# Optimization experiments

Hardware: AMD Instinct MI355X
Metric: run time of the kernel (lower is better)

Reference implementation:

```python
import jax, jax.numpy as jnp
import numpy as np

B, N, D = 8, 64, 512          # batch, latent tokens, token dim
C, H, W, P = 256, 128, 128, 36  # img feat channels/HW, sampling points
PG = 128                       # parameter-generator inner dim (0.25*D)
HEADS = 8                      # D // 64
TOT = C * C + P * P            # adaptive mixing param count per token


def _ln(x, g, b):
    m = x.mean(-1, keepdims=True)
    v = x.var(-1, keepdims=True)
    return (x - m) / jnp.sqrt(v + 1e-5) * g + b


def _gelu(x):
    return jax.nn.gelu(x, approximate=False)


def _grid_sample(img, grid):
    # img: (B,C,H,W); grid: (B,N,P,2) in [-1,1]; bilinear, border pad, align_corners=False
    Bi, Ci, Hi, Wi = img.shape
    x = ((grid[..., 0] + 1.0) * Wi - 1.0) * 0.5
    y = ((grid[..., 1] + 1.0) * Hi - 1.0) * 0.5
    x0 = jnp.floor(x)
    y0 = jnp.floor(y)
    wx = x - x0
    wy = y - y0
    x0i = jnp.clip(x0.astype(jnp.int32), 0, Wi - 1)
    x1i = jnp.clip(x0.astype(jnp.int32) + 1, 0, Wi - 1)
    y0i = jnp.clip(y0.astype(jnp.int32), 0, Hi - 1)
    y1i = jnp.clip(y0.astype(jnp.int32) + 1, 0, Hi - 1)
    imgt = img.transpose(0, 2, 3, 1)  # (B,H,W,C)
    bidx = jnp.arange(Bi)[:, None, None]
    v00 = imgt[bidx, y0i, x0i]  # (B,N,P,C)
    v01 = imgt[bidx, y0i, x1i]
    v10 = imgt[bidx, y1i, x0i]
    v11 = imgt[bidx, y1i, x1i]
    wx = wx[..., None]
    wy = wy[..., None]
    return (v00 * (1 - wx) * (1 - wy) + v01 * wx * (1 - wy)
            + v10 * (1 - wx) * wy + v11 * wx * wy)


def setup_inputs() -> dict:
    key = jax.random.key(0)
    ks = jax.random.split(key, 16)
    rn = lambda k, s, sc: jax.random.normal(k, s, jnp.float32) * sc
    tl = jax.random.uniform(ks[0], (B, N, 2), jnp.float32) * 0.5
    wh = 0.2 + jax.random.uniform(ks[1], (B, N, 2), jnp.float32) * 0.4
    return dict(
        token_embed=rn(ks[2], (B, N, D), 1.0),
        token_roi=jnp.concatenate([tl, tl + wh], axis=-1),
        img_feat=rn(ks[3], (B, C, H, W), 1.0),
        ln_off_g=jnp.ones(D), ln_off_b=jnp.zeros(D),
        w_off=rn(ks[4], (D, P * 2), D ** -0.5),
        roi_offset_bias=rn(ks[5], (P * 2,), 1.0),
        ln_pg_g=jnp.ones(D), ln_pg_b=jnp.zeros(D),
        w_pg1=rn(ks[6], (D, PG), D ** -0.5), b_pg1=jnp.zeros(PG),
        w_pg2=rn(ks[7], (PG, TOT), 0.02 * PG ** -0.5),
        b_pg2=rn(ks[8], (TOT,), 0.02),
        m_beta=jnp.zeros(C), s_beta=jnp.zeros(P),
        w_out=rn(ks[9], (P * C, D), (P * C) ** -0.5), b_out=jnp.zeros(D),
        ln1_g=jnp.ones(D), ln1_b=jnp.zeros(D),
        w_qkv=rn(ks[10], (D, 3 * D), D ** -0.5), b_qkv=jnp.zeros(3 * D),
        w_proj=rn(ks[11], (D, D), D ** -0.5), b_proj=jnp.zeros(D),
        ln2_g=jnp.ones(D), ln2_b=jnp.zeros(D),
        w_fc1=rn(ks[12], (D, 4 * D), D ** -0.5), b_fc1=jnp.zeros(4 * D),
        w_fc2=rn(ks[13], (4 * D, D), (4 * D) ** -0.5), b_fc2=jnp.zeros(D),
    )


def reference(token_embed, token_roi, img_feat,
              ln_off_g, ln_off_b, w_off, roi_offset_bias,
              ln_pg_g, ln_pg_b, w_pg1, b_pg1, w_pg2, b_pg2,
              m_beta, s_beta, w_out, b_out,
              ln1_g, ln1_b, w_qkv, b_qkv, w_proj, b_proj,
              ln2_g, ln2_b, w_fc1, b_fc1, w_fc2, b_fc2):
    Bq, Nq, Dm = token_embed.shape
    # --- OP.SAMPLING_M: offsets -> absolute points (n_heads=1) ---
    off = _ln(token_embed, ln_off_g, ln_off_b) @ w_off + roi_offset_bias  # (B,N,2P)
    off = off.reshape(Bq, Nq, 1, P, 2)
    mu = off.mean(-2, keepdims=True)
    sd = jnp.std(off, axis=-2, keepdims=True, ddof=1) + 1e-5  # unbiased, as torch.std
    off = (off - mu) / (3.0 * sd)
    xy = (token_roi[..., 2:] + token_roi[..., :2]) * 0.5
    wh = token_roi[..., 2:] - token_roi[..., :2]
    pts = xy[:, :, None, None, :] + off * wh[:, :, None, None, :]  # (B,N,1,P,2)
    grid = pts.reshape(Bq, Nq, P, 2) * 2.0 - 1.0
    sampled = _grid_sample(img_feat, grid)  # (B,N,P,C)
    # --- adaptive mixing (AdaMixer): per-token generated channel/spatial weights ---
    q = _ln(token_embed, ln_pg_g, ln_pg_b)
    params = (q @ w_pg1 + b_pg1) @ w_pg2 + b_pg2  # (B,N,TOT)
    cm = params[..., :C * C].reshape(Bq, Nq, C, C)
    sm = params[..., C * C:].reshape(Bq, Nq, P, P)
    h = _gelu(jnp.einsum('bnpc,bncd->bnpd', sampled, cm) + m_beta)
    h = _gelu(jnp.einsum('bnqp,bnpd->bnqd', sm, h) + s_beta[:, None])
    token_embed = token_embed + (h.reshape(Bq, Nq, P * C) @ w_out + b_out)
    # --- OP.ATTN ---
    x = _ln(token_embed, ln1_g, ln1_b)
    hd = Dm // HEADS
    qkv = (x @ w_qkv + b_qkv).reshape(Bq, Nq, 3, HEADS, hd)
    qh, kh, vh = qkv[:, :, 0], qkv[:, :, 1], qkv[:, :, 2]
    att = jax.nn.softmax(jnp.einsum('bqhd,bkhd->bhqk', qh, kh) * hd ** -0.5, axis=-1)
    o = jnp.einsum('bhqk,bkhd->bqhd', att, vh).reshape(Bq, Nq, Dm)
    token_embed = token_embed + (o @ w_proj + b_proj)
    # --- OP.MLP ---
    x = _ln(token_embed, ln2_g, ln2_b)
    token_embed = token_embed + (_gelu(x @ w_fc1 + b_fc1) @ w_fc2 + b_fc2)
    return token_embed
```

## Files before the change

### kernel.cpp

```cpp
#include <hip/hip_runtime.h>
#include <hip/hip_bf16.h>

typedef __hip_bfloat16 bf16;
typedef __attribute__((ext_vector_type(8))) short short8;
typedef __attribute__((ext_vector_type(4))) short s16x4;
typedef __attribute__((ext_vector_type(4))) float f32x4;

#define NTOK 512
#define TOTC 66832
#define CM_SZ 65536

__device__ __forceinline__ float b2f(bf16 x) { return __bfloat162float(x); }
__device__ __forceinline__ bf16 f2b(float x) { return __float2bfloat16(x); }
__device__ __forceinline__ float gelu_f(float x) {
  return 0.5f * x * (1.0f + erff(x * 0.7071067811865476f));
}
__device__ __forceinline__ f32x4 mfma16(short8 a, short8 b, f32x4 c) {
  return __builtin_amdgcn_mfma_f32_16x16x32_bf16(a, b, c, 0, 0, 0);
}

__global__ __launch_bounds__(256) void k_head(
    const float* __restrict__ te, const float* __restrict__ roi,
    const float* __restrict__ g_off, const float* __restrict__ b_off,
    const float* __restrict__ w_off, const float* __restrict__ off_bias,
    const float* __restrict__ g_pg, const float* __restrict__ b_pg,
    const float* __restrict__ w_pg1, const float* __restrict__ b_pg1,
    bf16* __restrict__ t_out, int* __restrict__ meta_i, float* __restrict__ meta_w,
    const float* __restrict__ img, bf16* __restrict__ imgT,
    const float* __restrict__ w0, bf16* __restrict__ o0,
    const float* __restrict__ w1, bf16* __restrict__ o1,
    const float* __restrict__ w2, bf16* __restrict__ o2,
    const float* __restrict__ w3, bf16* __restrict__ o3,
    const float* __restrict__ w4, bf16* __restrict__ o4) {
  __shared__ __align__(16) char smem_raw[36864];
  int blk = blockIdx.x;
  int t = threadIdx.x;
  if (blk < 512) {
    int tok = blk;
    int lane = t & 63, w = t >> 6;
    float* xo = (float*)smem_raw;
    float* xq = xo + 512;
    float* offb = xq + 512;
    float* red = offb + 72;
    float* wsum = red + 4;
    size_t base = (size_t)tok * 512;
    float a0 = te[base + t];
    float a1 = te[base + t + 256];
    float s = a0 + a1;
#pragma unroll
    for (int o = 32; o; o >>= 1) s += __shfl_xor(s, o);
    if (lane == 0) wsum[w] = s;
    __syncthreads();
    float mean = (wsum[0] + wsum[1] + wsum[2] + wsum[3]) * (1.0f / 512.0f);
    float d0 = a0 - mean, d1 = a1 - mean;
    float ss = d0 * d0 + d1 * d1;
#pragma unroll
    for (int o = 32; o; o >>= 1) ss += __shfl_xor(ss, o);
    __syncthreads();
    if (lane == 0) wsum[w] = ss;
    __syncthreads();
    float var = (wsum[0] + wsum[1] + wsum[2] + wsum[3]) * (1.0f / 512.0f);
    float rstd = rsqrtf(var + 1e-5f);
    xo[t] = d0 * rstd * g_off[t] + b_off[t];
    xo[t + 256] = d1 * rstd * g_off[t + 256] + b_off[t + 256];
    xq[t] = d0 * rstd * g_pg[t] + b_pg[t];
    xq[t + 256] = d1 * rstd * g_pg[t + 256] + b_pg[t + 256];
    __syncthreads();
    if (t < 128) {
      float acc = b_pg1[t];
      for (int d = 0; d < 512; ++d) acc = fmaf(xq[d], w_pg1[d * 128 + t], acc);
      t_out[(size_t)tok * 128 + t] = f2b(acc);
    } else if (t < 200) {
      int j = t - 128;
      float acc = off_bias[j];
      for (int d = 0; d < 512; ++d) acc = fmaf(xo[d], w_off[d * 72 + j], acc);
      offb[j] = acc;
    }
    __syncthreads();
    if (t < 2) {
      float mu = 0.f;
      for (int p = 0; p < 36; ++p) mu += offb[p * 2 + t];
      mu *= (1.0f / 36.0f);
      float s2 = 0.f;
      for (int p = 0; p < 36; ++p) { float dd = offb[p * 2 + t] - mu; s2 += dd * dd; }
      float sd = sqrtf(s2 * (1.0f / 35.0f)) + 1e-5f;
      red[t] = mu;
      red[2 + t] = 1.0f / (3.0f * sd);
    }
    __syncthreads();
    if (t < 36) {
      int p = t;
      float r0 = roi[tok * 4 + 0], r1 = roi[tok * 4 + 1];
      float r2 = roi[tok * 4 + 2], r3 = roi[tok * 4 + 3];
      float cx = (r0 + r2) * 0.5f, cy = (r1 + r3) * 0.5f;
      float bw = r2 - r0, bh = r3 - r1;
      float ox = (offb[p * 2 + 0] - red[0]) * red[2];
      float oy = (offb[p * 2 + 1] - red[1]) * red[3];
      float fx = (cx + ox * bw) * 128.0f - 0.5f;
      float fy = (cy + oy * bh) * 128.0f - 0.5f;
      float x0f = floorf(fx), y0f = floorf(fy);
      float wx = fx - x0f, wy = fy - y0f;
      int x0 = min(max((int)x0f, 0), 127);
      int x1 = min(max((int)x0f + 1, 0), 127);
      int y0 = min(max((int)y0f, 0), 127);
      int y1 = min(max((int)y0f + 1, 0), 127);
      int ibase = (tok >> 6) * 16384;
      int mi = (tok * 36 + p) * 4;
      meta_i[mi + 0] = (ibase + y0 * 128 + x0) * 256;
      meta_i[mi + 1] = (ibase + y0 * 128 + x1) * 256;
      meta_i[mi + 2] = (ibase + y1 * 128 + x0) * 256;
      meta_i[mi + 3] = (ibase + y1 * 128 + x1) * 256;
      meta_w[mi + 0] = (1.f - wx) * (1.f - wy);
      meta_w[mi + 1] = wx * (1.f - wy);
      meta_w[mi + 2] = (1.f - wx) * wy;
      meta_w[mi + 3] = wx * wy;
    }
  } else if (blk < 2560) {
    int bb = blk - 512;
    int b = bb >> 8;
    int hw0 = (bb & 255) * 64;
    bf16 (*tl)[72] = (bf16(*)[72])smem_raw;
    int hw_l = (t & 15) * 4;
#pragma unroll
    for (int pass = 0; pass < 16; ++pass) {
      int c = (t >> 4) + 16 * pass;
      const float4 v = *(const float4*)&img[((size_t)(b * 256 + c) << 14) + hw0 + hw_l];
      float vv[4] = {v.x, v.y, v.z, v.w};
      int mask = ((c >> 3) & 31) << 1;
      int base = hw_l ^ (mask & 60);
      int swp = mask & 2;
      bf16 o[4];
#pragma unroll
      for (int k = 0; k < 4; ++k) o[k] = f2b(vv[k ^ swp]);
      *(s16x4*)&tl[c][base] = *(const s16x4*)o;
    }
    __syncthreads();
    int c8 = (t & 31) * 8;
    int hwb = t >> 5;
    int rmask = ((c8 >> 3) & 31) << 1;
#pragma unroll
    for (int pass = 0; pass < 8; ++pass) {
      int hw = hwb + 8 * pass;
      bf16 tmp[8];
#pragma unroll
      for (int j = 0; j < 8; ++j) tmp[j] = tl[c8 + j][hw ^ rmask];
      *(short8*)&imgT[((size_t)(b << 14) + hw0 + hw) * 256 + c8] = *(const short8*)tmp;
    }
  } else {
    int b = blk - 2560;
    const float* W;
    bf16* O;
    int K, N, loc;
    if (b < 4608) { W = w0; O = o0; K = 9216; N = 512; loc = b; }
    else if (b < 5376) { W = w1; O = o1; K = 512; N = 1536; loc = b - 4608; }
    else if (b < 5632) { W = w2; O = o2; K = 512; N = 512; loc = b - 5376; }
    else if (b < 6656) { W = w3; O = o3; K = 512; N = 2048; loc = b - 5632; }
    else { W = w4; O = o4; K = 2048; N = 512; loc = b - 6656; }
    int ntn = N >> 5;
    int nb = loc % ntn, kb = loc / ntn;
    int n0 = nb * 32, k0 = kb * 32;
    float (*tw)[33] = (float(*)[33])smem_raw;
    int r = t >> 5, c = t & 31;
#pragma unroll
    for (int i = 0; i < 4; ++i)
      tw[r + 8 * i][c] = W[(size_t)(k0 + r + 8 * i) * N + n0 + c];
    __syncthreads();
    int n_l = t >> 3, k4 = (t & 7) * 4;
    bf16 tmp[4];
#pragma unroll
    for (int j = 0; j < 4; ++j) tmp[j] = f2b(tw[k4 + j][n_l]);
    *(s16x4*)&O[(size_t)(n0 + n_l) * K + k0 + k4] = *(const s16x4*)tmp;
  }
}

__global__ __launch_bounds__(256) void k_samp_pg2(
    const bf16* __restrict__ tb16, const float* __restrict__ w2,
    const float* __restrict__ b2, bf16* __restrict__ pchunk,
    const bf16* __restrict__ imgT, const int* __restrict__ meta_i,
    const float* __restrict__ meta_w, bf16* __restrict__ S) {
  __shared__ bf16 BsT[64][136];
  __shared__ bf16 stg[64][72];
  int blk = blockIdx.x;
  int t = threadIdx.x;
  if (blk < 1045) {
    int n0 = blk * 64;
    int lane = t & 63, w = t >> 6;
    int quad = lane >> 4, l16 = lane & 15;
    {
      int nl = (t & 15) * 4, kk = t >> 4;
#pragma unroll
      for (int pass = 0; pass < 8; ++pass) {
        int k = kk + pass * 16;
        int n = n0 + nl;
        int nc = (n + 3 < TOTC) ? n : (TOTC - 4);
        const float4 v = *(const float4*)(w2 + (size_t)k * TOTC + nc);
        BsT[nl + 0][k] = f2b(v.x);
        BsT[nl + 1][k] = f2b(v.y);
        BsT[nl + 2][k] = f2b(v.z);
        BsT[nl + 3][k] = f2b(v.w);
      }
    }
    __syncthreads();
    float bias_r[4];
#pragma unroll
    for (int nt = 0; nt < 4; ++nt) {
      int col = n0 + nt * 16 + l16;
      bias_r[nt] = (col < TOTC) ? b2[col] : 0.f;
    }
    for (int half = 0; half < 2; ++half) {
      int row0 = half * 256;
      f32x4 acc[4][4];
#pragma unroll
      for (int i = 0; i < 4; ++i)
#pragma unroll
        for (int j = 0; j < 4; ++j) acc[i][j] = (f32x4){0.f, 0.f, 0.f, 0.f};
      const bf16* Abase = tb16 + ((size_t)(row0 + w * 64 + l16)) * 128 + quad * 8;
#pragma unroll
      for (int ks = 0; ks < 4; ++ks) {
        short8 af[4], bff[4];
#pragma unroll
        for (int mt = 0; mt < 4; ++mt)
          af[mt] = *(const short8*)(Abase + mt * 16 * 128 + ks * 32);
#pragma unroll
        for (int nt = 0; nt < 4; ++nt)
          bff[nt] = *(const short8*)(&BsT[nt * 16 + l16][ks * 32 + quad * 8]);
#pragma unroll
        for (int mt = 0; mt < 4; ++mt)
#pragma unroll
          for (int nt = 0; nt < 4; ++nt)
            acc[mt][nt] = mfma16(af[mt], bff[nt], acc[mt][nt]);
      }
#pragma unroll
      for (int mt = 0; mt < 4; ++mt) {
        __syncthreads();
#pragma unroll
        for (int nt = 0; nt < 4; ++nt)
#pragma unroll
          for (int r = 0; r < 4; ++r)
            stg[w * 16 + quad * 4 + r][nt * 16 + l16] =
                f2b(acc[mt][nt][r] + bias_r[nt]);
        __syncthreads();
#pragma unroll
        for (int pass = 0; pass < 2; ++pass) {
          int t2 = t + pass * 256;
          int row_l = t2 >> 3;
          int wi = row_l >> 4, rr = row_l & 15;
          int c8 = (t2 & 7) * 8;
          int col = n0 + c8;
          if (col < TOTC) {
            int grow = row0 + wi * 64 + mt * 16 + rr;
            *(short8*)&pchunk[(size_t)grow * TOTC + col] =
                *(const short8*)&stg[wi * 16 + rr][c8];
          }
        }
      }
      __syncthreads();
    }
  } else {
    int tok = blk - 1045;
#pragma unroll 6
    for (int p = 0; p < 36; ++p) {
      int mi = (tok * 36 + p) * 4;
      int o00 = meta_i[mi + 0], o01 = meta_i[mi + 1], o10 = meta_i[mi + 2], o11 = meta_i[mi + 3];
      float w00 = meta_w[mi + 0], w01 = meta_w[mi + 1], w10 = meta_w[mi + 2], w11 = meta_w[mi + 3];
      float v = w00 * b2f(imgT[o00 + t]) + w01 * b2f(imgT[o01 + t]) +
                w10 * b2f(imgT[o10 + t]) + w11 * b2f(imgT[o11 + t]);
      S[((size_t)tok * 36 + p) * 256 + t] = f2b(v);
    }
  }
}

__global__ __launch_bounds__(256) void k_mix3(const bf16* __restrict__ pchunk,
                                              const bf16* __restrict__ S,
                                              const float* __restrict__ m_beta,
                                              const float* __restrict__ s_beta,
                                              bf16* __restrict__ h2) {
  int tok = blockIdx.x, dh = blockIdx.y * 128;
  int t = threadIdx.x, lane = t & 63, w = t >> 6;
  int quad = lane >> 4, l16 = lane & 15;
  __shared__ bf16 h1T[128][72];
  __shared__ bf16 smS[48][72];
  __shared__ short cmw[4][32][40];
  for (int i = t; i < 1728; i += 256) ((unsigned*)smS)[i] = 0u;
  __syncthreads();
  const bf16* sm = pchunk + (size_t)tok * TOTC + CM_SZ;
  for (int i = t; i < 1296; i += 256) {
    int q = i / 36, p = i - q * 36;
    smS[q][p] = sm[i];
  }
  f32x4 acc[3][2];
#pragma unroll
  for (int i = 0; i < 3; ++i)
#pragma unroll
    for (int j = 0; j < 2; ++j) acc[i][j] = (f32x4){0.f, 0.f, 0.f, 0.f};
  const bf16* Sg = S + (size_t)tok * 9216;
  const bf16* Cg = pchunk + (size_t)tok * TOTC;
  int dw = w * 32;
  int c_l = lane & 31;
  int dtop = (lane >> 5) * 16;
  const bf16* src0 = Cg + (size_t)c_l * 256 + dh + dw + dtop;
  short8 v0 = *(const short8*)src0;
  short8 v1 = *(const short8*)(src0 + 8);
#pragma unroll
  for (int kc = 0; kc < 256; kc += 32) {
#pragma unroll
    for (int j = 0; j < 8; ++j) cmw[w][dtop + j][c_l] = v0[j];
#pragma unroll
    for (int j = 0; j < 8; ++j) cmw[w][dtop + 8 + j][c_l] = v1[j];
    short8 a[3];
#pragma unroll
    for (int mt = 0; mt < 3; ++mt)
      a[mt] = *(const short8*)(Sg + (size_t)(mt * 16 + l16) * 256 + kc + quad * 8);
    short8 v0n, v1n;
    if (kc < 224) {
      const bf16* srcn = Cg + (size_t)(kc + 32 + c_l) * 256 + dh + dw + dtop;
      v0n = *(const short8*)srcn;
      v1n = *(const short8*)(srcn + 8);
    }
    asm volatile("" ::: "memory");
    short8 bfr[2];
#pragma unroll
    for (int nt = 0; nt < 2; ++nt)
      bfr[nt] = *(const short8*)&cmw[w][nt * 16 + l16][quad * 8];
#pragma unroll
    for (int mt = 0; mt < 3; ++mt)
#pragma unroll
      for (int nt = 0; nt < 2; ++nt)
        acc[mt][nt] = mfma16(a[mt], bfr[nt], acc[mt][nt]);
    asm volatile("" ::: "memory");
    v0 = v0n;
    v1 = v1n;
  }
#pragma unroll
  for (int nt = 0; nt < 2; ++nt) {
    int dl = dw + nt * 16 + l16;
    float mb = m_beta[dh + dl];
#pragma unroll
    for (int mt = 0; mt < 3; ++mt)
#pragma unroll
      for (int r = 0; r < 4; ++r) {
        int p = mt * 16 + quad * 4 + r;
        if (p < 36) h1T[dl][p] = f2b(gelu_f(acc[mt][nt][r] + mb));
      }
  }
  for (int i = t; i < 128 * 28; i += 256) {
    int d = i / 28, p = 36 + i % 28;
    h1T[d][p] = (bf16)0.f;
  }
  __syncthreads();
  f32x4 acc2[3][2];
#pragma unroll
  for (int i = 0; i < 3; ++i)
#pragma unroll
    for (int j = 0; j < 2; ++j) acc2[i][j] = (f32x4){0.f, 0.f, 0.f, 0.f};
#pragma unroll
  for (int ks = 0; ks < 2; ++ks) {
    short8 a2[3], b2v[2];
#pragma unroll
    for (int mt = 0; mt < 3; ++mt)
      a2[mt] = *(const short8*)&smS[mt * 16 + l16][ks * 32 + quad * 8];
#pragma unroll
    for (int nt = 0; nt < 2; ++nt)
      b2v[nt] = *(const short8*)&h1T[dw + nt * 16 + l16][ks * 32 + quad * 8];
#pragma unroll
    for (int mt = 0; mt < 3; ++mt)
#pragma unroll
      for (int nt = 0; nt < 2; ++nt)
        acc2[mt][nt] = mfma16(a2[mt], b2v[nt], acc2[mt][nt]);
  }
  bf16* h2p = h2 + (size_t)tok * 9216 + dh;
#pragma unroll
  for (int mt = 0; mt < 3; ++mt)
#pragma unroll
    for (int r = 0; r < 4; ++r) {
      int q = mt * 16 + quad * 4 + r;
      if (q >= 36) continue;
      float sb = s_beta[q];
#pragma unroll
      for (int nt = 0; nt < 2; ++nt)
        h2p[q * 256 + dw + nt * 16 + l16] = f2b(gelu_f(acc2[mt][nt][r] + sb));
    }
}

__global__ __launch_bounds__(256) void k_gemm_bt(const bf16* __restrict__ A,
                                                 const bf16* __restrict__ BT,
                                                 float* __restrict__ part,
                                                 int M, int N, int K) {
  int nb = blockIdx.x, mb = blockIdx.y, ks = blockIdx.z;
  int kchunk = K / gridDim.z;
  int k0 = ks * kchunk;
  __shared__ bf16 As[64][72], Bs[64][72];
  int t = threadIdx.x, lane = t & 63, w = t >> 6;
  int quad = lane >> 4, l16 = lane & 15;
  int wm = (w >> 1) * 32, wn = (w & 1) * 32;
  int r = t >> 2, kk = (t & 3) * 16;
  f32x4 acc[2][2];
#pragma unroll
  for (int i = 0; i < 2; ++i)
#pragma unroll
    for (int j = 0; j < 2; ++j) acc[i][j] = (f32x4){0.f, 0.f, 0.f, 0.f};
  for (int kt = 0; kt < kchunk; kt += 64) {
    __syncthreads();
    const bf16* ga = A + (size_t)(mb * 64 + r) * K + k0 + kt + kk;
    *(short8*)&As[r][kk] = *(const short8*)ga;
    *(short8*)&As[r][kk + 8] = *(const short8*)(ga + 8);
    const bf16* gb = BT + (size_t)(nb * 64 + r) * K + k0 + kt + kk;
    *(short8*)&Bs[r][kk] = *(const short8*)gb;
    *(short8*)&Bs[r][kk + 8] = *(const short8*)(gb + 8);
    __syncthreads();
#pragma unroll
    for (int kss = 0; kss < 2; ++kss) {
      short8 af[2], bff[2];
#pragma unroll
      for (int mt = 0; mt < 2; ++mt)
        af[mt] = *(const short8*)&As[wm + mt * 16 + l16][kss * 32 + quad * 8];
#pragma unroll
      for (int nt = 0; nt < 2; ++nt)
        bff[nt] = *(const short8*)&Bs[wn + nt * 16 + l16][kss * 32 + quad * 8];
#pragma unroll
      for (int mt = 0; mt < 2; ++mt)
#pragma unroll
        for (int nt = 0; nt < 2; ++nt)
          acc[mt][nt] = mfma16(af[mt], bff[nt], acc[mt][nt]);
    }
  }
#pragma unroll
  for (int mt = 0; mt < 2; ++mt)
#pragma unroll
    for (int rr = 0; rr < 4; ++rr) {
      int m = mb * 64 + wm + mt * 16 + quad * 4 + rr;
#pragma unroll
      for (int nt = 0; nt < 2; ++nt) {
        int n = nb * 64 + wn + nt * 16 + l16;
        part[(size_t)ks * M * N + (size_t)m * N + n] = acc[mt][nt][rr];
      }
    }
}

__global__ __launch_bounds__(256) void k_gemm_ep(const bf16* __restrict__ A,
                                                 const bf16* __restrict__ BT,
                                                 const float* __restrict__ bias,
                                                 int M, int N, int K, int do_gelu,
                                                 const float* __restrict__ resf,
                                                 float* __restrict__ outf,
                                                 bf16* __restrict__ outh) {
  int nb = blockIdx.x, mb = blockIdx.y;
  __shared__ bf16 As[64][72], Bs[64][72];
  int t = threadIdx.x, lane = t & 63, w = t >> 6;
  int quad = lane >> 4, l16 = lane & 15;
  int wm = (w >> 1) * 32, wn = (w & 1) * 32;
  int r = t >> 2, kk = (t & 3) * 16;
  f32x4 acc[2][2];
#pragma unroll
  for (int i = 0; i < 2; ++i)
#pragma unroll
    for (int j = 0; j < 2; ++j) acc[i][j] = (f32x4){0.f, 0.f, 0.f, 0.f};
  for (int kt = 0; kt < K; kt += 64) {
    __syncthreads();
    const bf16* ga = A + (size_t)(mb * 64 + r) * K + kt + kk;
    *(short8*)&As[r][kk] = *(const short8*)ga;
    *(short8*)&As[r][kk + 8] = *(const short8*)(ga + 8);
    const bf16* gb = BT + (size_t)(nb * 64 + r) * K + kt + kk;
    *(short8*)&Bs[r][kk] = *(const short8*)gb;
    *(short8*)&Bs[r][kk + 8] = *(const short8*)(gb + 8);
    __syncthreads();
#pragma unroll
    for (int kss = 0; kss < 2; ++kss) {
      short8 af[2], bff[2];
#pragma unroll
      for (int mt = 0; mt < 2; ++mt)
        af[mt] = *(const short8*)&As[wm + mt * 16 + l16][kss * 32 + quad * 8];
#pragma unroll
      for (int nt = 0; nt < 2; ++nt)
        bff[nt] = *(const short8*)&Bs[wn + nt * 16 + l16][kss * 32 + quad * 8];
#pragma unroll
      for (int mt = 0; mt < 2; ++mt)
#pragma unroll
        for (int nt = 0; nt < 2; ++nt)
          acc[mt][nt] = mfma16(af[mt], bff[nt], acc[mt][nt]);
    }
  }
#pragma unroll
  for (int mt = 0; mt < 2; ++mt)
#pragma unroll
    for (int rr = 0; rr < 4; ++rr) {
      int m = mb * 64 + wm + mt * 16 + quad * 4 + rr;
#pragma unroll
      for (int nt = 0; nt < 2; ++nt) {
        int n = nb * 64 + wn + nt * 16 + l16;
        float a = acc[mt][nt][rr] + bias[n];
        if (resf) a += resf[(size_t)m * N + n];
        if (do_gelu) a = gelu_f(a);
        if (outf) outf[(size_t)m * N + n] = a;
        else outh[(size_t)m * N + n] = f2b(a);
      }
    }
}

__global__ __launch_bounds__(256) void k_epi_ln(const float* __restrict__ part, int S_,
                                                const float* __restrict__ bias,
                                                const float* __restrict__ res,
                                                const float* __restrict__ g,
                                                const float* __restrict__ bvec,
                                                float* __restrict__ xout,
                                                bf16* __restrict__ lnout) {
  int tok = blockIdx.x, t = threadIdx.x, lane = t & 63, w = t >> 6;
  __shared__ float wsum[4];
  size_t base = (size_t)tok * 512;
  float a0 = bias[t] + res[base + t];
  float a1 = bias[t + 256] + res[base + t + 256];
  for (int sp = 0; sp < S_; ++sp) {
    const float* p = part + (size_t)sp * 262144 + base;
    a0 += p[t];
    a1 += p[t + 256];
  }
  xout[base + t] = a0;
  xout[base + t + 256] = a1;
  float s = a0 + a1;
#pragma unroll
  for (int o = 32; o; o >>= 1) s += __shfl_xor(s, o);
  if (lane == 0) wsum[w] = s;
  __syncthreads();
  float mean = (wsum[0] + wsum[1] + wsum[2] + wsum[3]) * (1.0f / 512.0f);
  float d0 = a0 - mean, d1 = a1 - mean;
  float ss = d0 * d0 + d1 * d1;
#pragma unroll
  for (int o = 32; o; o >>= 1) ss += __shfl_xor(ss, o);
  __syncthreads();
  if (lane == 0) wsum[w] = ss;
  __syncthreads();
  float var = (wsum[0] + wsum[1] + wsum[2] + wsum[3]) * (1.0f / 512.0f);
  float rstd = rsqrtf(var + 1e-5f);
  lnout[base + t] = f2b(d0 * rstd * g[t] + bvec[t]);
  lnout[base + t + 256] = f2b(d1 * rstd * g[t + 256] + bvec[t + 256]);
}

__global__ __launch_bounds__(256) void k_attn(const float* __restrict__ qkvf,
                                              bf16* __restrict__ obuf) {
  int b = blockIdx.x >> 3, h = blockIdx.x & 7;
  int q0 = blockIdx.y * 16;
  __shared__ float kT[64][65];
  __shared__ float vT[64][65];
  __shared__ float att[16][65];
  int t = threadIdx.x, lane = t & 63, w = t >> 6;
#pragma unroll
  for (int i = 0; i < 16; ++i) {
    int idx = t + i * 256;
    int j = idx >> 6, d = idx & 63;
    size_t tb = (size_t)(b * 64 + j) * 1536 + h * 64 + d;
    kT[j][d] = qkvf[tb + 512];
    vT[j][d] = qkvf[tb + 1024];
  }
  __syncthreads();
#pragma unroll
  for (int m = 0; m < 4; ++m) {
    int il = w * 4 + m;
    int i = q0 + il;
    const float* qrow = &qkvf[(size_t)(b * 64 + i) * 1536 + h * 64];
    float s = 0.f;
    for (int d = 0; d < 64; ++d) s = fmaf(qrow[d], kT[lane][d], s);
    s *= 0.125f;
    float mx = s;
#pragma unroll
    for (int o = 32; o; o >>= 1) mx = fmaxf(mx, __shfl_xor(mx, o));
    float e = expf(s - mx);
    float sum = e;
#pragma unroll
    for (int o = 32; o; o >>= 1) sum += __shfl_xor(sum, o);
    att[il][lane] = e / sum;
  }
  __syncthreads();
#pragma unroll
  for (int m = 0; m < 4; ++m) {
    int il = w * 4 + m;
    int i = q0 + il;
    float o = 0.f;
    for (int j = 0; j < 64; ++j) o = fmaf(att[il][j], vT[j][lane], o);
    obuf[(size_t)(b * 64 + i) * 512 + h * 64 + lane] = f2b(o);
  }
}

extern "C" void kernel_launch(void* const* d_in, const int* in_sizes, int n_in,
                              void* d_out, int out_size, void* d_ws, size_t ws_size,
                              hipStream_t stream) {
  const float* te = (const float*)d_in[0];
  const float* roi = (const float*)d_in[1];
  const float* img = (const float*)d_in[2];
  const float* ln_off_g = (const float*)d_in[3];
  const float* ln_off_b = (const float*)d_in[4];
  const float* w_off = (const float*)d_in[5];
  const float* off_bias = (const float*)d_in[6];
  const float* ln_pg_g = (const float*)d_in[7];
  const float* ln_pg_b = (const float*)d_in[8];
  const float* w_pg1 = (const float*)d_in[9];
  const float* b_pg1 = (const float*)d_in[10];
  const float* w_pg2 = (const float*)d_in[11];
  const float* b_pg2 = (const float*)d_in[12];
  const float* m_beta = (const float*)d_in[13];
  const float* s_beta = (const float*)d_in[14];
  const float* w_out = (const float*)d_in[15];
  const float* b_out = (const float*)d_in[16];
  const float* ln1_g = (const float*)d_in[17];
  const float* ln1_b = (const float*)d_in[18];
  const float* w_qkv = (const float*)d_in[19];
  const float* b_qkv = (const float*)d_in[20];
  const float* w_proj = (const float*)d_in[21];
  const float* b_proj = (const float*)d_in[22];
  const float* ln2_g = (const float*)d_in[23];
  const float* ln2_b = (const float*)d_in[24];
  const float* w_fc1 = (const float*)d_in[25];
  const float* b_fc1 = (const float*)d_in[26];
  const float* w_fc2 = (const float*)d_in[27];
  const float* b_fc2 = (const float*)d_in[28];

  char* ws = (char*)d_ws;
  bf16* imgT = (bf16*)ws;
  char* ov = ws;
  bf16* h2 = (bf16*)ov; ov += 9437184;
  float* part = (float*)ov; ov += 8388608;
  float* x1 = (float*)ov; ov += 1048576;
  float* xa = (float*)ov; ov += 1048576;
  float* qkvf = (float*)ov; ov += 3145728;
  bf16* ln1buf = (bf16*)ov; ov += 524288;
  bf16* ln2buf = (bf16*)ov; ov += 524288;
  bf16* obuf = (bf16*)ov; ov += 524288;
  bf16* hfc = (bf16*)ov; ov += 2097152;
  char* tail = ws + 67108864;
  bf16* Sbuf = (bf16*)tail; tail += 9437184;
  bf16* tb16 = (bf16*)tail; tail += 131072;
  int* meta_i = (int*)tail; tail += 294912;
  float* meta_w = (float*)tail; tail += 294912;
  bf16* pchunk = (bf16*)tail; tail += (size_t)NTOK * TOTC * 2;
  bf16* w_outT = (bf16*)tail; tail += 9437184;
  bf16* w_qkvT = (bf16*)tail; tail += 1572864;
  bf16* w_projT = (bf16*)tail; tail += 524288;
  bf16* w_fc1T = (bf16*)tail; tail += 2097152;
  bf16* w_fc2T = (bf16*)tail; tail += 2097152;
  (void)ws_size;

  k_head<<<10240, 256, 0, stream>>>(te, roi, ln_off_g, ln_off_b, w_off, off_bias,
                                    ln_pg_g, ln_pg_b, w_pg1, b_pg1, tb16, meta_i, meta_w,
                                    img, imgT,
                                    w_out, w_outT, w_qkv, w_qkvT, w_proj, w_projT,
                                    w_fc1, w_fc1T, w_fc2, w_fc2T);
  k_samp_pg2<<<1557, 256, 0, stream>>>(tb16, w_pg2, b_pg2, pchunk,
                                       imgT, meta_i, meta_w, Sbuf);
  k_mix3<<<dim3(512, 2), 256, 0, stream>>>(pchunk, Sbuf, m_beta, s_beta, h2);

  k_gemm_bt<<<dim3(8, 8, 8), 256, 0, stream>>>(h2, w_outT, part, 512, 512, 9216);
  k_epi_ln<<<512, 256, 0, stream>>>(part, 8, b_out, te, ln1_g, ln1_b, x1, ln1buf);

  k_gemm_ep<<<dim3(24, 8), 256, 0, stream>>>(ln1buf, w_qkvT, b_qkv, 512, 1536, 512, 0,
                                             nullptr, qkvf, nullptr);
  k_attn<<<dim3(64, 4), 256, 0, stream>>>(qkvf, obuf);
  k_gemm_bt<<<dim3(8, 8, 4), 256, 0, stream>>>(obuf, w_projT, part, 512, 512, 512);
  k_epi_ln<<<512, 256, 0, stream>>>(part, 4, b_proj, x1, ln2_g, ln2_b, xa, ln2buf);

  k_gemm_ep<<<dim3(32, 8), 256, 0, stream>>>(ln2buf, w_fc1T, b_fc1, 512, 2048, 512, 1,
                                             nullptr, nullptr, hfc);
  k_gemm_ep<<<dim3(8, 8), 256, 0, stream>>>(hfc, w_fc2T, b_fc2, 512, 512, 2048, 0,
                                            xa, (float*)d_out, nullptr);
}
```

Baseline: 487.4 us.

## Split image transpose into its own kernel and split-K the final FC2 GEMM

Moves the NCHW-to-NHWC bf16 image transpose out of the fused head kernel into a dedicated 1024-thread kernel with a 256x256 shared tile. This lets the head kernel drop its large shared-memory buffer, which should raise occupancy for the LN and weight-transpose blocks. The FC2 GEMM (K=2048, only 64 blocks) is changed to a split-K GEMM writing partials, followed by a new elementwise epilogue kernel that adds bias and residual. The cost is an extra kernel launch and an extra round trip of the partial sums through memory.

```diff
diff --git a/kernel.cpp b/kernel.cpp
--- a/kernel.cpp
+++ b/kernel.cpp
@@ -17,6 +17,40 @@
 }
 __device__ __forceinline__ f32x4 mfma16(short8 a, short8 b, f32x4 c) {
   return __builtin_amdgcn_mfma_f32_16x16x32_bf16(a, b, c, 0, 0, 0);
+}
+
+__global__ __launch_bounds__(1024) void k_imgT(const float* __restrict__ img,
+                                               bf16* __restrict__ imgT) {
+  __shared__ bf16 tl[256][256];
+  int t = threadIdx.x;
+  int b = blockIdx.y;
+  int hw0 = blockIdx.x * 256;
+  int lane4 = (t & 63) * 4;
+#pragma unroll
+  for (int pass = 0; pass < 16; ++pass) {
+    int c = (t >> 6) + 16 * pass;
+    const float4 v = *(const float4*)&img[((size_t)(b * 256 + c) << 14) + hw0 + lane4];
+    float vv[4] = {v.x, v.y, v.z, v.w};
+    int mask = ((c >> 3) & 31) << 1;
+    int base = lane4 ^ (mask & 60);
+    int swp = mask & 2;
+    bf16 o[4];
+#pragma unroll
+    for (int k = 0; k < 4; ++k) o[k] = f2b(vv[k ^ swp]);
+    *(s16x4*)&tl[c][base] = *(const s16x4*)o;
+  }
+  __syncthreads();
+  int c8 = (t & 31) * 8;
+  int hwb = t >> 5;
+  int rmask = ((c8 >> 3) & 31) << 1;
+#pragma unroll
+  for (int pass = 0; pass < 8; ++pass) {
+    int hw = hwb + 32 * pass;
+    bf16 tmp[8];
+#pragma unroll
+    for (int j = 0; j < 8; ++j) tmp[j] = tl[c8 + j][hw ^ rmask];
+    *(short8*)&imgT[((size_t)(b << 14) + hw0 + hw) * 256 + c8] = *(const short8*)tmp;
+  }
 }
 
 __global__ __launch_bounds__(256) void k_head(
@@ -26,13 +60,12 @@
     const float* __restrict__ g_pg, const float* __restrict__ b_pg,
     const float* __restrict__ w_pg1, const float* __restrict__ b_pg1,
     bf16* __restrict__ t_out, int* __restrict__ meta_i, float* __restrict__ meta_w,
-    const float* __restrict__ img, bf16* __restrict__ imgT,
     const float* __restrict__ w0, bf16* __restrict__ o0,
     const float* __restrict__ w1, bf16* __restrict__ o1,
     const float* __restrict__ w2, bf16* __restrict__ o2,
     const float* __restrict__ w3, bf16* __restrict__ o3,
     const float* __restrict__ w4, bf16* __restrict__ o4) {
-  __shared__ __align__(16) char smem_raw[36864];
+  __shared__ __align__(16) char smem_raw[4608];
   int blk = blockIdx.x;
   int t = threadIdx.x;
   if (blk < 512) {
@@ -40,9 +73,12 @@
     int lane = t & 63, w = t >> 6;
     float* xo = (float*)smem_raw;
     float* xq = xo + 512;
-    float* offb = xq + 512;
+    __shared__ float xtra[1152];
+    float* xq2 = xtra;
+    float* offb = xtra + 512;
     float* red = offb + 72;
     float* wsum = red + 4;
+    (void)xq;
     size_t base = (size_t)tok * 512;
     float a0 = te[base + t];
     float a1 = te[base + t + 256];
@@ -63,12 +99,12 @@
     float rstd = rsqrtf(var + 1e-5f);
     xo[t] = d0 * rstd * g_off[t] + b_off[t];
     xo[t + 256] = d1 * rstd * g_off[t + 256] + b_off[t + 256];
-    xq[t] = d0 * rstd * g_pg[t] + b_pg[t];
-    xq[t + 256] = d1 * rstd * g_pg[t + 256] + b_pg[t + 256];
+    xq2[t] = d0 * rstd * g_pg[t] + b_pg[t];
+    xq2[t + 256] = d1 * rstd * g_pg[t + 256] + b_pg[t + 256];
     __syncthreads();
     if (t < 128) {
       float acc = b_pg1[t];
-      for (int d = 0; d < 512; ++d) acc = fmaf(xq[d], w_pg1[d * 128 + t], acc);
+      for (int d = 0; d < 512; ++d) acc = fmaf(xq2[d], w_pg1[d * 128 + t], acc);
       t_out[(size_t)tok * 128 + t] = f2b(acc);
     } else if (t < 200) {
       int j = t - 128;
@@ -115,39 +151,8 @@
       meta_w[mi + 2] = (1.f - wx) * wy;
       meta_w[mi + 3] = wx * wy;
     }
-  } else if (blk < 2560) {
-    int bb = blk - 512;
-    int b = bb >> 8;
-    int hw0 = (bb & 255) * 64;
-    bf16 (*tl)[72] = (bf16(*)[72])smem_raw;
-    int hw_l = (t & 15) * 4;
-#pragma unroll
-    for (int pass = 0; pass < 16; ++pass) {
-      int c = (t >> 4) + 16 * pass;
-      const float4 v = *(const float4*)&img[((size_t)(b * 256 + c) << 14) + hw0 + hw_l];
-      float vv[4] = {v.x, v.y, v.z, v.w};
-      int mask = ((c >> 3) & 31) << 1;
-      int base = hw_l ^ (mask & 60);
-      int swp = mask & 2;
-      bf16 o[4];
-#pragma unroll
-      for (int k = 0; k < 4; ++k) o[k] = f2b(vv[k ^ swp]);
-      *(s16x4*)&tl[c][base] = *(const s16x4*)o;
-    }
-    __syncthreads();
-    int c8 = (t & 31) * 8;
-    int hwb = t >> 5;
-    int rmask = ((c8 >> 3) & 31) << 1;
-#pragma unroll
-    for (int pass = 0; pass < 8; ++pass) {
-      int hw = hwb + 8 * pass;
-      bf16 tmp[8];
-#pragma unroll
-      for (int j = 0; j < 8; ++j) tmp[j] = tl[c8 + j][hw ^ rmask];
-      *(short8*)&imgT[((size_t)(b << 14) + hw0 + hw) * 256 + c8] = *(const short8*)tmp;
-    }
   } else {
-    int b = blk - 2560;
+    int b = blk - 512;
     const float* W;
     bf16* O;
     int K, N, loc;
@@ -495,6 +500,22 @@
         else outh[(size_t)m * N + n] = f2b(a);
       }
     }
+}
+
+__global__ __launch_bounds__(256) void k_epi(const float* __restrict__ part, int S_,
+                                             int MN, int N, const float* __restrict__ bias,
+                                             const float* __restrict__ resf, int do_gelu,
+                                             float* __restrict__ outf, bf16* __restrict__ outh) {
+  int idx = blockIdx.x * 256 + threadIdx.x;
+  if (idx >= MN) return;
+  int n = idx % N;
+  float a = 0.f;
+  for (int s = 0; s < S_; ++s) a += part[(size_t)s * MN + idx];
+  a += bias[n];
+  if (resf) a += resf[idx];
+  if (do_gelu) a = gelu_f(a);
+  if (outf) outf[idx] = a;
+  if (outh) outh[idx] = f2b(a);
 }
 
 __global__ __launch_bounds__(256) void k_epi_ln(const float* __restrict__ part, int S_,
@@ -638,11 +659,11 @@
   bf16* w_fc2T = (bf16*)tail; tail += 2097152;
   (void)ws_size;
 
-  k_head<<<10240, 256, 0, stream>>>(te, roi, ln_off_g, ln_off_b, w_off, off_bias,
-                                    ln_pg_g, ln_pg_b, w_pg1, b_pg1, tb16, meta_i, meta_w,
-                                    img, imgT,
-                                    w_out, w_outT, w_qkv, w_qkvT, w_proj, w_projT,
-                                    w_fc1, w_fc1T, w_fc2, w_fc2T);
+  k_imgT<<<dim3(64, 8), 1024, 0, stream>>>(img, imgT);
+  k_head<<<8192, 256, 0, stream>>>(te, roi, ln_off_g, ln_off_b, w_off, off_bias,
+                                   ln_pg_g, ln_pg_b, w_pg1, b_pg1, tb16, meta_i, meta_w,
+                                   w_out, w_outT, w_qkv, w_qkvT, w_proj, w_projT,
+                                   w_fc1, w_fc1T, w_fc2, w_fc2T);
   k_samp_pg2<<<1557, 256, 0, stream>>>(tb16, w_pg2, b_pg2, pchunk,
                                        imgT, meta_i, meta_w, Sbuf);
   k_mix3<<<dim3(512, 2), 256, 0, stream>>>(pchunk, Sbuf, m_beta, s_beta, h2);
@@ -658,6 +679,6 @@
 
   k_gemm_ep<<<dim3(32, 8), 256, 0, stream>>>(ln2buf, w_fc1T, b_fc1, 512, 2048, 512, 1,
                                              nullptr, nullptr, hfc);
-  k_gemm_ep<<<dim3(8, 8), 256, 0, stream>>>(hfc, w_fc2T, b_fc2, 512, 512, 2048, 0,
-                                            xa, (float*)d_out, nullptr);
-}
+  k_gemm_bt<<<dim3(8, 8, 4), 256, 0, stream>>>(hfc, w_fc2T, part, 512, 512, 2048);
+  k_epi<<<1024, 256, 0, stream>>>(part, 4, 512 * 512, 512, b_fc2, xa, 0, (float*)d_out, nullptr);
+}
```

Measured after the change: 490.4 us. About the same (+0.6%).
